# Kernel tuning notes

Hardware: AMD Instinct MI355X
Metric: run time of the kernel (lower is better)

## Reference

```python
import jax, jax.numpy as jnp
from jax import lax
import numpy as np


def _lstm(x, h0, c0, Wih, Whh, bih, bhh):
    """Single-layer batch-first LSTM, PyTorch gate order (i, f, g, o).
    x: [B, T, I]; h0, c0: [B, H]. Returns (outputs [B, T, H], h_n [B, H], c_n [B, H])."""
    # Precompute input projections for all timesteps in one GEMM.
    xg = jnp.einsum('bti,gi->btg', x, Wih) + (bih + bhh)  # [B, T, 4H]
    H = h0.shape[-1]

    def step(carry, xt):
        h, c = carry
        gates = xt + h @ Whh.T  # [B, 4H]
        i, f, g, o = jnp.split(gates, 4, axis=-1)
        i = jax.nn.sigmoid(i)
        f = jax.nn.sigmoid(f)
        g = jnp.tanh(g)
        o = jax.nn.sigmoid(o)
        c = f * c + i * g
        h = o * jnp.tanh(c)
        return (h, c), h

    (h_n, c_n), hs = lax.scan(step, (h0, c0), jnp.swapaxes(xg, 0, 1))
    return jnp.swapaxes(hs, 0, 1), h_n, c_n


def setup_inputs() -> dict:
    key = jax.random.key(0)
    B, T, I, H, L = 4096, 512, 25, 20, 10
    ks = jax.random.split(key, 20)
    p = lambda k, shp: (jax.random.normal(k, shp, dtype=jnp.float32) * 0.1)
    return {
        'input_filters': jax.random.normal(ks[0], (B, T, I), dtype=jnp.float32),
        'h0': jnp.zeros((1, B, H), dtype=jnp.float32),
        'c0': jnp.zeros((1, B, H), dtype=jnp.float32),
        'noise': jax.random.normal(ks[1], (B, L), dtype=jnp.float32),
        'enc_Wih': p(ks[2], (4 * H, I)), 'enc_Whh': p(ks[3], (4 * H, H)),
        'enc_bih': p(ks[4], (4 * H,)), 'enc_bhh': p(ks[5], (4 * H,)),
        'dec_Wih': p(ks[6], (4 * H, I)), 'dec_Whh': p(ks[7], (4 * H, H)),
        'dec_bih': p(ks[8], (4 * H,)), 'dec_bhh': p(ks[9], (4 * H,)),
        'mean_W': p(ks[10], (L, H)), 'mean_b': p(ks[11], (L,)),
        'logvar_W': p(ks[12], (L, H)), 'logvar_b': p(ks[13], (L,)),
        'init_W': p(ks[14], (H, L)), 'init_b': p(ks[15], (H,)),
        'out_W': p(ks[16], (I, H)), 'out_b': p(ks[17], (I,)),
    }


def reference(input_filters, h0, c0, noise,
              enc_Wih, enc_Whh, enc_bih, enc_bhh,
              dec_Wih, dec_Whh, dec_bih, dec_bhh,
              mean_W, mean_b, logvar_W, logvar_b,
              init_W, init_b, out_W, out_b):
    # Encoder LSTM (num_layers == 1, squeeze the layer dim of h0/c0)
    _, h_n, c_n = _lstm(input_filters, h0[0], c0[0], enc_Wih, enc_Whh, enc_bih, enc_bhh)
    # mean / log_var from final hidden state, reparameterize
    mean = h_n @ mean_W.T + mean_b          # [B, L]
    log_var = h_n @ logvar_W.T + logvar_b   # [B, L]
    std = jnp.exp(0.5 * log_var)
    z = noise * std + mean                  # [B, L]
    # Decoder: z -> initial (h, c); teacher-forced decoder over same inputs
    hd = z @ init_W.T + init_b              # [B, H]
    out_dec, _, _ = _lstm(input_filters, hd, hd, dec_Wih, dec_Whh, dec_bih, dec_bhh)
    x_hat = jnp.einsum('bth,oh->bto', out_dec, out_W) + out_b  # [B, T, I]
    # Match torch shapes: mean/log_var/z carry num_layers leading dim
    return (x_hat, mean[None], log_var[None], z[None], h_n[None], c_n[None])
```

## Files before the change

### kernel.cpp

```cpp
#include <hip/hip_runtime.h>

#define NB 4096
#define NT 512
#define NI 25
#define NH 20
#define NL 10

#if __has_builtin(__builtin_amdgcn_rcpf)
__device__ __forceinline__ float rcpf(float x){ return __builtin_amdgcn_rcpf(x); }
#else
__device__ __forceinline__ float rcpf(float x){ return 1.0f/x; }
#endif

struct Smem {
  float xbuf[4][28];
  float hbuf[4][20];
  float gbuf[4][80];
  float zbuf[4][12];
};

__device__ __forceinline__ void load_wb(const float* __restrict__ Wih, const float* __restrict__ Whh,
                                        const float* __restrict__ bih, const float* __restrict__ bhh,
                                        int k, float (&wih)[5][25], float (&whh)[5][20], float (&bias)[5])
{
#pragma unroll
  for (int g=0; g<5; ++g){
    const int G = 5*k+g;
#pragma unroll
    for (int i=0;i<25;++i) wih[g][i] = Wih[G*25+i];
#pragma unroll
    for (int j=0;j<20;++j) whh[g][j] = Whh[G*20+j];
    bias[g] = bih[G] + bhh[G];
  }
}

template<bool DEC>
__device__ __forceinline__ void lstm_phase(
    const float* __restrict__ xrowbase,
    Smem* sm, int r, int k,
    const float (&wih)[5][25], const float (&whh)[5][20], const float (&bias)[5],
    float (&c)[2],
    const float (&ow)[2][20], const float (&obias)[2],
    float* __restrict__ xhat_out)
{
  const bool is_g = ((k>>2)==2);
  const float gmul = is_g ? -2.0f : -1.0f;
  float u0 = xrowbase[k];
  float u1 = (k<9) ? xrowbase[16+k] : 0.0f;
  for (int t=0; t<NT; ++t){
    sm->xbuf[r][k] = u0;
    if (k<9) sm->xbuf[r][16+k] = u1;
    if (t+1 < NT){
      const float* xr = xrowbase + (size_t)(t+1)*NI;
      u0 = xr[k];
      if (k<9) u1 = xr[16+k];
    }
    __syncthreads();
    float xreg[25], hreg[20];
#pragma unroll
    for (int i=0;i<25;++i) xreg[i] = sm->xbuf[r][i];
#pragma unroll
    for (int j=0;j<20;++j) hreg[j] = sm->hbuf[r][j];

    if (DEC && t>0 && k<13){
      float a0 = obias[0];
#pragma unroll
      for (int j=0;j<20;++j) a0 = fmaf(ow[0][j], hreg[j], a0);
      xhat_out[(size_t)(t-1)*NI + k] = a0;
      if (k<12){
        float a1 = obias[1];
#pragma unroll
        for (int j=0;j<20;++j) a1 = fmaf(ow[1][j], hreg[j], a1);
        xhat_out[(size_t)(t-1)*NI + 13 + k] = a1;
      }
    }

    float acc[5];
#pragma unroll
    for (int g=0; g<5; ++g) acc[g]=bias[g];
#pragma unroll
    for (int i=0;i<25;++i){
      const float xv = xreg[i];
#pragma unroll
      for (int g=0;g<5;++g) acc[g] = fmaf(wih[g][i], xv, acc[g]);
    }
#pragma unroll
    for (int j=0;j<20;++j){
      const float hv = hreg[j];
#pragma unroll
      for (int g=0;g<5;++g) acc[g] = fmaf(whh[g][j], hv, acc[g]);
    }
#pragma unroll
    for (int g=0; g<5; ++g){
      float e = __expf(gmul*acc[g]);
      float s = rcpf(1.0f + e);
      float res = is_g ? (2.0f*s - 1.0f) : s;
      sm->gbuf[r][5*k+g] = res;
    }
    __syncthreads();
    {
      float ii = sm->gbuf[r][k], ff = sm->gbuf[r][k+20], gg = sm->gbuf[r][k+40], oo = sm->gbuf[r][k+60];
      float cn = fmaf(ff, c[0], ii*gg);
      c[0] = cn;
      float e = __expf(-2.0f*cn);
      float th = 2.0f*rcpf(1.0f + e) - 1.0f;
      sm->hbuf[r][k] = oo*th;
      if (k<4){
        float i2 = sm->gbuf[r][16+k], f2_ = sm->gbuf[r][36+k], g2 = sm->gbuf[r][56+k], o2 = sm->gbuf[r][76+k];
        float cn2 = fmaf(f2_, c[1], i2*g2);
        c[1] = cn2;
        float e2 = __expf(-2.0f*cn2);
        float th2 = 2.0f*rcpf(1.0f + e2) - 1.0f;
        sm->hbuf[r][16+k] = o2*th2;
      }
    }
  }
}

__global__ __launch_bounds__(64,1) void lstm_vae_kernel(
  const float* __restrict__ x, const float* __restrict__ h0, const float* __restrict__ c0,
  const float* __restrict__ noise,
  const float* __restrict__ eWih, const float* __restrict__ eWhh, const float* __restrict__ ebih, const float* __restrict__ ebhh,
  const float* __restrict__ dWih, const float* __restrict__ dWhh, const float* __restrict__ dbih, const float* __restrict__ dbhh,
  const float* __restrict__ mW, const float* __restrict__ mb,
  const float* __restrict__ lW, const float* __restrict__ lb,
  const float* __restrict__ iW, const float* __restrict__ ib,
  const float* __restrict__ oW, const float* __restrict__ ob,
  float* __restrict__ out)
{
  __shared__ Smem sm;
  const int lane = threadIdx.x;
  const int r = lane>>4, k = lane&15;
  const int b = blockIdx.x*4 + r;
  const float* xrow = x + (size_t)b*NT*NI;

  float wih[5][25], whh[5][20], bias[5];
  float ow[2][20], obias[2];
  float c[2] = {0.f, 0.f};

  sm.hbuf[r][k] = h0[(size_t)b*NH + k];
  c[0] = c0[(size_t)b*NH + k];
  if (k<4){
    sm.hbuf[r][16+k] = h0[(size_t)b*NH + 16+k];
    c[1] = c0[(size_t)b*NH + 16+k];
  }

  load_wb(eWih, eWhh, ebih, ebhh, k, wih, whh, bias);
  lstm_phase<false>(xrow, &sm, r, k, wih, whh, bias, c, ow, obias, nullptr);

  __syncthreads();
  float hT[20];
#pragma unroll
  for (int j=0;j<20;++j) hT[j] = sm.hbuf[r][j];

  const size_t OFF1 = (size_t)NB*NT*NI;
  const size_t OFF2 = OFF1 + (size_t)NB*NL;
  const size_t OFF3 = OFF2 + (size_t)NB*NL;
  const size_t OFF4 = OFF3 + (size_t)NB*NL;
  const size_t OFF5 = OFF4 + (size_t)NB*NH;

  out[OFF4 + (size_t)b*NH + k] = hT[k];
  out[OFF5 + (size_t)b*NH + k] = c[0];
  if (k<4){
    out[OFF4 + (size_t)b*NH + 16+k] = hT[16+k];
    out[OFF5 + (size_t)b*NH + 16+k] = c[1];
  }

  if (k<10){
    float m = mb[k], lv = lb[k];
#pragma unroll
    for (int j=0;j<20;++j){
      m  = fmaf(mW[k*20+j], hT[j], m);
      lv = fmaf(lW[k*20+j], hT[j], lv);
    }
    float sd = __expf(0.5f*lv);
    float zz = fmaf(noise[(size_t)b*NL + k], sd, m);
    out[OFF1 + (size_t)b*NL + k] = m;
    out[OFF2 + (size_t)b*NL + k] = lv;
    out[OFF3 + (size_t)b*NL + k] = zz;
    sm.zbuf[r][k] = zz;
  }
  __syncthreads();
  {
    float hd = ib[k];
#pragma unroll
    for (int l=0;l<10;++l) hd = fmaf(iW[k*10+l], sm.zbuf[r][l], hd);
    sm.hbuf[r][k] = hd; c[0] = hd;
    if (k<4){
      float hd2 = ib[16+k];
#pragma unroll
      for (int l=0;l<10;++l) hd2 = fmaf(iW[(16+k)*10+l], sm.zbuf[r][l], hd2);
      sm.hbuf[r][16+k] = hd2; c[1] = hd2;
    }
  }

  load_wb(dWih, dWhh, dbih, dbhh, k, wih, whh, bias);
  if (k<13){
#pragma unroll
    for (int j=0;j<20;++j) ow[0][j] = oW[k*20+j];
    obias[0] = ob[k];
    if (k<12){
#pragma unroll
      for (int j=0;j<20;++j) ow[1][j] = oW[(13+k)*20+j];
      obias[1] = ob[13+k];
    }
  }
  float* xhat = out + (size_t)b*NT*NI;
  lstm_phase<true>(xrow, &sm, r, k, wih, whh, bias, c, ow, obias, xhat);

  __syncthreads();
#pragma unroll
  for (int j=0;j<20;++j) hT[j] = sm.hbuf[r][j];
  if (k<13){
    float a0 = obias[0];
#pragma unroll
    for (int j=0;j<20;++j) a0 = fmaf(ow[0][j], hT[j], a0);
    xhat[(size_t)(NT-1)*NI + k] = a0;
    if (k<12){
      float a1 = obias[1];
#pragma unroll
      for (int j=0;j<20;++j) a1 = fmaf(ow[1][j], hT[j], a1);
      xhat[(size_t)(NT-1)*NI + 13+k] = a1;
    }
  }
}

extern "C" void kernel_launch(void* const* d_in, const int* in_sizes, int n_in,
                              void* d_out, int out_size, void* d_ws, size_t ws_size,
                              hipStream_t stream) {
  const float* x     = (const float*)d_in[0];
  const float* h0    = (const float*)d_in[1];
  const float* c0    = (const float*)d_in[2];
  const float* noise = (const float*)d_in[3];
  const float* eWih  = (const float*)d_in[4];
  const float* eWhh  = (const float*)d_in[5];
  const float* ebih  = (const float*)d_in[6];
  const float* ebhh  = (const float*)d_in[7];
  const float* dWih  = (const float*)d_in[8];
  const float* dWhh  = (const float*)d_in[9];
  const float* dbih  = (const float*)d_in[10];
  const float* dbhh  = (const float*)d_in[11];
  const float* mW    = (const float*)d_in[12];
  const float* mb    = (const float*)d_in[13];
  const float* lW    = (const float*)d_in[14];
  const float* lb    = (const float*)d_in[15];
  const float* iW    = (const float*)d_in[16];
  const float* ib    = (const float*)d_in[17];
  const float* oW    = (const float*)d_in[18];
  const float* ob    = (const float*)d_in[19];
  float* out = (float*)d_out;

  hipLaunchKernelGGL(lstm_vae_kernel, dim3(NB/4), dim3(64), 0, stream,
                     x, h0, c0, noise,
                     eWih, eWhh, ebih, ebhh,
                     dWih, dWhh, dbih, dbhh,
                     mW, mb, lW, lb, iW, ib, oW, ob, out);
}
```

Measured before the change: 997.7 us.

## Split LSTM gate matvec across half-waves and stage input chunks in LDS

```diff
diff --git a/kernel.cpp b/kernel.cpp
--- a/kernel.cpp
+++ b/kernel.cpp
@@ -5,6 +5,9 @@
 #define NI 25
 #define NH 20
 #define NL 10
+#define CH 32
+
+typedef float f4 __attribute__((ext_vector_type(4)));
 
 #if __has_builtin(__builtin_amdgcn_rcpf)
 __device__ __forceinline__ float rcpf(float x){ return __builtin_amdgcn_rcpf(x); }
@@ -13,111 +16,132 @@
 #endif
 
 struct Smem {
-  float xbuf[4][28];
-  float hbuf[4][20];
-  float gbuf[4][80];
-  float zbuf[4][12];
+  float xbuf[2][CH][32];
+  float hbuf[2][32];
+  float gbuf[2][128];
+  float zbuf[2][12];
 };
 
-__device__ __forceinline__ void load_wb(const float* __restrict__ Wih, const float* __restrict__ Whh,
-                                        const float* __restrict__ bih, const float* __restrict__ bhh,
-                                        int k, float (&wih)[5][25], float (&whh)[5][20], float (&bias)[5])
+__device__ __forceinline__ void load_weights(
+    const float* __restrict__ Wih, const float* __restrict__ Whh,
+    const float* __restrict__ bih, const float* __restrict__ bhh,
+    int p, int k, float (&w)[5][25], float (&bias)[5])
 {
 #pragma unroll
   for (int g=0; g<5; ++g){
     const int G = 5*k+g;
-#pragma unroll
-    for (int i=0;i<25;++i) wih[g][i] = Wih[G*25+i];
-#pragma unroll
-    for (int j=0;j<20;++j) whh[g][j] = Whh[G*20+j];
-    bias[g] = bih[G] + bhh[G];
+    if (p==0){
+#pragma unroll
+      for (int i=0;i<25;++i) w[g][i] = Wih[G*25+i];
+      bias[g] = bih[G] + bhh[G];
+    } else {
+#pragma unroll
+      for (int j=0;j<20;++j) w[g][j] = Whh[G*20+j];
+#pragma unroll
+      for (int j=20;j<25;++j) w[g][j] = 0.f;
+      bias[g] = 0.f;
+    }
   }
 }
 
 template<bool DEC>
-__device__ __forceinline__ void lstm_phase(
-    const float* __restrict__ xrowbase,
-    Smem* sm, int r, int k,
-    const float (&wih)[5][25], const float (&whh)[5][20], const float (&bias)[5],
-    float (&c)[2],
-    const float (&ow)[2][20], const float (&obias)[2],
-    float* __restrict__ xhat_out)
+__device__ __forceinline__ void lstm_loop(
+    const float* __restrict__ xblk,
+    Smem* sm, int lane, int r, int p, int k,
+    const float (&w)[5][25], const float (&bias)[5],
+    float& c,
+    const float (&ow)[20], float obias,
+    float* __restrict__ xhat)
 {
   const bool is_g = ((k>>2)==2);
   const float gmul = is_g ? -2.0f : -1.0f;
-  float u0 = xrowbase[k];
-  float u1 = (k<9) ? xrowbase[16+k] : 0.0f;
+  const bool upd = (p==0) || (k<4);
+  const int  m   = (p==0) ? k : 16+k;
+  const int  ai  = (m/5)*8 + (m%5);
+  const int  q2  = lane & 31;
+  const bool pj  = (q2 < 25);
+  const float* opbase = (p==0) ? &sm->xbuf[r][0][0] : &sm->hbuf[r][0];
+
   for (int t=0; t<NT; ++t){
-    sm->xbuf[r][k] = u0;
-    if (k<9) sm->xbuf[r][16+k] = u1;
-    if (t+1 < NT){
-      const float* xr = xrowbase + (size_t)(t+1)*NI;
-      u0 = xr[k];
-      if (k<9) u1 = xr[16+k];
-    }
-    __syncthreads();
-    float xreg[25], hreg[20];
-#pragma unroll
-    for (int i=0;i<25;++i) xreg[i] = sm->xbuf[r][i];
-#pragma unroll
-    for (int j=0;j<20;++j) hreg[j] = sm->hbuf[r][j];
-
-    if (DEC && t>0 && k<13){
-      float a0 = obias[0];
-#pragma unroll
-      for (int j=0;j<20;++j) a0 = fmaf(ow[0][j], hreg[j], a0);
-      xhat_out[(size_t)(t-1)*NI + k] = a0;
-      if (k<12){
-        float a1 = obias[1];
-#pragma unroll
-        for (int j=0;j<20;++j) a1 = fmaf(ow[1][j], hreg[j], a1);
-        xhat_out[(size_t)(t-1)*NI + 13 + k] = a1;
+    const int tc = t & (CH-1);
+    if (tc == 0){
+      __syncthreads();
+      const float* gsrc = xblk + (size_t)t*NI;
+#pragma unroll
+      for (int it=0; it<25; ++it){
+        int idx = lane + it*64;
+        int rr  = (idx >= 800) ? 1 : 0;
+        int o   = idx - rr*800;
+        int tt  = o / 25;
+        int ii  = o - tt*25;
+        sm->xbuf[rr][tt][ii] = gsrc[(size_t)rr*NT*NI + (size_t)tt*NI + ii];
       }
+      __syncthreads();
+    }
+
+    const float* obp = (p==0) ? (opbase + tc*32) : opbase;
+    float op[28];
+#pragma unroll
+    for (int v=0; v<7; ++v){
+      f4 q = *(const f4*)(obp + 4*v);
+      op[4*v+0]=q.x; op[4*v+1]=q.y; op[4*v+2]=q.z; op[4*v+3]=q.w;
     }
 
     float acc[5];
 #pragma unroll
-    for (int g=0; g<5; ++g) acc[g]=bias[g];
+    for (int g=0; g<5; ++g) acc[g] = (p==0) ? bias[g] : 0.f;
 #pragma unroll
     for (int i=0;i<25;++i){
-      const float xv = xreg[i];
-#pragma unroll
-      for (int g=0;g<5;++g) acc[g] = fmaf(wih[g][i], xv, acc[g]);
-    }
-#pragma unroll
-    for (int j=0;j<20;++j){
-      const float hv = hreg[j];
-#pragma unroll
-      for (int g=0;g<5;++g) acc[g] = fmaf(whh[g][j], hv, acc[g]);
-    }
+      const float xv = op[i];
+#pragma unroll
+      for (int g=0;g<5;++g) acc[g] = fmaf(w[g][i], xv, acc[g]);
+    }
+#pragma unroll
+    for (int g=0; g<5; ++g) acc[g] += __shfl_xor(acc[g], 16);
+
+    float val[5];
 #pragma unroll
     for (int g=0; g<5; ++g){
       float e = __expf(gmul*acc[g]);
       float s = rcpf(1.0f + e);
-      float res = is_g ? (2.0f*s - 1.0f) : s;
-      sm->gbuf[r][5*k+g] = res;
+      val[g] = is_g ? (2.0f*s - 1.0f) : s;
+    }
+    if (p==0){
+      f4 v4; v4.x=val[0]; v4.y=val[1]; v4.z=val[2]; v4.w=val[3];
+      *(f4*)&sm->gbuf[r][k*8] = v4;
+      sm->gbuf[r][k*8+4] = val[4];
     }
     __syncthreads();
-    {
-      float ii = sm->gbuf[r][k], ff = sm->gbuf[r][k+20], gg = sm->gbuf[r][k+40], oo = sm->gbuf[r][k+60];
-      float cn = fmaf(ff, c[0], ii*gg);
-      c[0] = cn;
-      float e = __expf(-2.0f*cn);
+
+    if (upd){
+      float ig = sm->gbuf[r][ai];
+      float fg = sm->gbuf[r][ai+32];
+      float gg = sm->gbuf[r][ai+64];
+      float og = sm->gbuf[r][ai+96];
+      float cn = fmaf(fg, c, ig*gg);
+      c = cn;
+      float e  = __expf(-2.0f*cn);
       float th = 2.0f*rcpf(1.0f + e) - 1.0f;
-      sm->hbuf[r][k] = oo*th;
-      if (k<4){
-        float i2 = sm->gbuf[r][16+k], f2_ = sm->gbuf[r][36+k], g2 = sm->gbuf[r][56+k], o2 = sm->gbuf[r][76+k];
-        float cn2 = fmaf(f2_, c[1], i2*g2);
-        c[1] = cn2;
-        float e2 = __expf(-2.0f*cn2);
-        float th2 = 2.0f*rcpf(1.0f + e2) - 1.0f;
-        sm->hbuf[r][16+k] = o2*th2;
+      sm->hbuf[r][m] = og*th;
+    }
+    __syncthreads();
+
+    if (DEC && pj){
+      float h[20];
+#pragma unroll
+      for (int v=0; v<5; ++v){
+        f4 q = *(const f4*)(&sm->hbuf[r][4*v]);
+        h[4*v+0]=q.x; h[4*v+1]=q.y; h[4*v+2]=q.z; h[4*v+3]=q.w;
       }
-    }
-  }
-}
-
-__global__ __launch_bounds__(64,1) void lstm_vae_kernel(
+      float a = obias;
+#pragma unroll
+      for (int j=0;j<20;++j) a = fmaf(ow[j], h[j], a);
+      xhat[(size_t)t*NI] = a;
+    }
+  }
+}
+
+__global__ __launch_bounds__(64,2) void lstm_vae_kernel(
   const float* __restrict__ x, const float* __restrict__ h0, const float* __restrict__ c0,
   const float* __restrict__ noise,
   const float* __restrict__ eWih, const float* __restrict__ eWhh, const float* __restrict__ ebih, const float* __restrict__ ebhh,
@@ -130,28 +154,29 @@
 {
   __shared__ Smem sm;
   const int lane = threadIdx.x;
-  const int r = lane>>4, k = lane&15;
-  const int b = blockIdx.x*4 + r;
-  const float* xrow = x + (size_t)b*NT*NI;
-
-  float wih[5][25], whh[5][20], bias[5];
-  float ow[2][20], obias[2];
-  float c[2] = {0.f, 0.f};
-
-  sm.hbuf[r][k] = h0[(size_t)b*NH + k];
-  c[0] = c0[(size_t)b*NH + k];
-  if (k<4){
-    sm.hbuf[r][16+k] = h0[(size_t)b*NH + 16+k];
-    c[1] = c0[(size_t)b*NH + 16+k];
-  }
-
-  load_wb(eWih, eWhh, ebih, ebhh, k, wih, whh, bias);
-  lstm_phase<false>(xrow, &sm, r, k, wih, whh, bias, c, ow, obias, nullptr);
-
-  __syncthreads();
-  float hT[20];
-#pragma unroll
-  for (int j=0;j<20;++j) hT[j] = sm.hbuf[r][j];
+  const int r = lane>>5, p = (lane>>4)&1, k = lane&15;
+  const int b = blockIdx.x*2 + r;
+  const bool upd = (p==0) || (k<4);
+  const int  m   = (p==0) ? k : 16+k;
+  const float* xblk = x + (size_t)(blockIdx.x*2)*NT*NI;
+
+  ((float*)sm.hbuf)[lane] = 0.f;
+  float c = 0.f;
+  __syncthreads();
+  if (upd){
+    sm.hbuf[r][m] = h0[(size_t)b*NH + m];
+    c = c0[(size_t)b*NH + m];
+  }
+
+  float w[5][25], bias[5];
+  load_weights(eWih, eWhh, ebih, ebhh, p, k, w, bias);
+  float ow[20]; float obias = 0.f;
+#pragma unroll
+  for (int j=0;j<20;++j) ow[j] = 0.f;
+  __syncthreads();
+
+  lstm_loop<false>(xblk, &sm, lane, r, p, k, w, bias, c, ow, obias, nullptr);
+  __syncthreads();
 
   const size_t OFF1 = (size_t)NB*NT*NI;
   const size_t OFF2 = OFF1 + (size_t)NB*NL;
@@ -159,70 +184,49 @@
   const size_t OFF4 = OFF3 + (size_t)NB*NL;
   const size_t OFF5 = OFF4 + (size_t)NB*NH;
 
-  out[OFF4 + (size_t)b*NH + k] = hT[k];
-  out[OFF5 + (size_t)b*NH + k] = c[0];
-  if (k<4){
-    out[OFF4 + (size_t)b*NH + 16+k] = hT[16+k];
-    out[OFF5 + (size_t)b*NH + 16+k] = c[1];
-  }
-
-  if (k<10){
-    float m = mb[k], lv = lb[k];
+  if (upd){
+    out[OFF4 + (size_t)b*NH + m] = sm.hbuf[r][m];
+    out[OFF5 + (size_t)b*NH + m] = c;
+  }
+
+  if (p==0 && k<10){
+    float h[20];
+#pragma unroll
+    for (int j=0;j<20;++j) h[j] = sm.hbuf[r][j];
+    float mm = mb[k], lv = lb[k];
 #pragma unroll
     for (int j=0;j<20;++j){
-      m  = fmaf(mW[k*20+j], hT[j], m);
-      lv = fmaf(lW[k*20+j], hT[j], lv);
+      mm = fmaf(mW[k*20+j], h[j], mm);
+      lv = fmaf(lW[k*20+j], h[j], lv);
     }
     float sd = __expf(0.5f*lv);
-    float zz = fmaf(noise[(size_t)b*NL + k], sd, m);
-    out[OFF1 + (size_t)b*NL + k] = m;
+    float zz = fmaf(noise[(size_t)b*NL + k], sd, mm);
+    out[OFF1 + (size_t)b*NL + k] = mm;
     out[OFF2 + (size_t)b*NL + k] = lv;
     out[OFF3 + (size_t)b*NL + k] = zz;
     sm.zbuf[r][k] = zz;
   }
   __syncthreads();
-  {
-    float hd = ib[k];
-#pragma unroll
-    for (int l=0;l<10;++l) hd = fmaf(iW[k*10+l], sm.zbuf[r][l], hd);
-    sm.hbuf[r][k] = hd; c[0] = hd;
-    if (k<4){
-      float hd2 = ib[16+k];
-#pragma unroll
-      for (int l=0;l<10;++l) hd2 = fmaf(iW[(16+k)*10+l], sm.zbuf[r][l], hd2);
-      sm.hbuf[r][16+k] = hd2; c[1] = hd2;
-    }
-  }
-
-  load_wb(dWih, dWhh, dbih, dbhh, k, wih, whh, bias);
-  if (k<13){
-#pragma unroll
-    for (int j=0;j<20;++j) ow[0][j] = oW[k*20+j];
-    obias[0] = ob[k];
-    if (k<12){
-#pragma unroll
-      for (int j=0;j<20;++j) ow[1][j] = oW[(13+k)*20+j];
-      obias[1] = ob[13+k];
-    }
-  }
-  float* xhat = out + (size_t)b*NT*NI;
-  lstm_phase<true>(xrow, &sm, r, k, wih, whh, bias, c, ow, obias, xhat);
-
-  __syncthreads();
-#pragma unroll
-  for (int j=0;j<20;++j) hT[j] = sm.hbuf[r][j];
-  if (k<13){
-    float a0 = obias[0];
-#pragma unroll
-    for (int j=0;j<20;++j) a0 = fmaf(ow[0][j], hT[j], a0);
-    xhat[(size_t)(NT-1)*NI + k] = a0;
-    if (k<12){
-      float a1 = obias[1];
-#pragma unroll
-      for (int j=0;j<20;++j) a1 = fmaf(ow[1][j], hT[j], a1);
-      xhat[(size_t)(NT-1)*NI + 13+k] = a1;
-    }
-  }
+
+  if (upd){
+    float hd = ib[m];
+#pragma unroll
+    for (int l=0;l<10;++l) hd = fmaf(iW[m*10+l], sm.zbuf[r][l], hd);
+    c = hd;
+    sm.hbuf[r][m] = hd;
+  }
+
+  load_weights(dWih, dWhh, dbih, dbhh, p, k, w, bias);
+  const int q2 = lane & 31;
+  if (q2 < 25){
+#pragma unroll
+    for (int j=0;j<20;++j) ow[j] = oW[q2*20+j];
+    obias = ob[q2];
+  }
+  float* xhat = out + (size_t)b*NT*NI + q2;
+  __syncthreads();
+
+  lstm_loop<true>(xblk, &sm, lane, r, p, k, w, bias, c, ow, obias, xhat);
 }
 
 extern "C" void kernel_launch(void* const* d_in, const int* in_sizes, int n_in,
@@ -250,7 +254,7 @@
   const float* ob    = (const float*)d_in[19];
   float* out = (float*)d_out;
 
-  hipLaunchKernelGGL(lstm_vae_kernel, dim3(NB/4), dim3(64), 0, stream,
+  hipLaunchKernelGGL(lstm_vae_kernel, dim3(NB/2), dim3(64), 0, stream,
                      x, h0, c0, noise,
                      eWih, eWhh, ebih, ebhh,
                      dWih, dWhh, dbih, dbhh,
```

Result: slower. 1.032 ms (+3.5%).
